# Kernel optimization log

Hardware: AMD Instinct MI355X
Metric: run time of the kernel (lower is better)

The kernel has to match this reference:

```python
import jax, jax.numpy as jnp
import numpy as np

B, CIN, COUT, H, W, K = 4, 64, 64, 128, 128, 3
KK = K * K


def setup_inputs() -> dict:
    key = jax.random.key(0)
    k = jax.random.split(key, 7)
    return {
        "input_feat": jax.random.normal(k[0], (B, CIN, H, W), jnp.float32),
        "inter": jax.random.normal(k[1], (B, CIN, H, W), jnp.float32),
        "fea": jax.random.normal(k[2], (B, 4 * CIN, 1, 1), jnp.float32),
        "weight": jax.random.uniform(k[3], (COUT, CIN, K, K), jnp.float32, -1.0, 1.0) / np.float32(np.sqrt(CIN * KK)),
        "bias": jnp.zeros((COUT,), jnp.float32),
        # conv_offset_mask params (torch zero-inits; small random values used so offsets/masks are non-trivial)
        "com_w": jax.random.normal(k[4], (3 * KK, CIN, K, K), jnp.float32) * 0.01,
        "com_b": jnp.zeros((3 * KK,), jnp.float32),
        "c1_w": jax.random.normal(k[5], (COUT, 4 * CIN), jnp.float32) / np.float32(np.sqrt(4 * CIN)),
        "c2_w": jax.random.normal(k[6], (COUT, COUT), jnp.float32) / np.float32(np.sqrt(COUT)),
    }


def reference(input_feat, inter, fea, weight, bias, com_w, com_b, c1_w, c2_w):
    b, c, h, w = input_feat.shape
    # offset/mask prediction: 3x3 conv, stride 1, pad 1 -> [b, 3*KK, h, w]
    om = jax.lax.conv_general_dilated(inter, com_w, (1, 1), ((1, 1), (1, 1)),
                                      dimension_numbers=("NCHW", "OIHW", "NCHW"))
    om = om + com_b[None, :, None, None]
    offset = jnp.concatenate([om[:, :KK], om[:, KK:2 * KK]], axis=1)  # [b, 2*KK, h, w]
    mask = jax.nn.sigmoid(om[:, 2 * KK:])                              # [b, KK, h, w]
    dy, dx = offset[:, 0::2], offset[:, 1::2]                          # mmcv interleaved (y, x) per tap

    # dynamic per-sample weight modulation (Cout == Cin, fea scales the in-channel axis)
    fvec = jnp.einsum('oc,bc->bo', c1_w, fea[:, :, 0, 0])              # [b, COUT]
    wdyn = weight[None] * fvec[:, None, :, None, None]                 # [b, COUT, CIN, K, K]

    # sampling coordinates: base grid (stride=1, pad=1, dil=1) + learned offsets
    ky = jnp.repeat(jnp.arange(K), K).astype(jnp.float32)              # [KK]
    kx = jnp.tile(jnp.arange(K), K).astype(jnp.float32)
    base_y = jnp.arange(h, dtype=jnp.float32)[None, :, None] - 1.0 + ky[:, None, None]  # [KK, h, 1]
    base_x = jnp.arange(w, dtype=jnp.float32)[None, None, :] - 1.0 + kx[:, None, None]  # [KK, 1, w]
    ys = base_y[None] + dy                                             # [b, KK, h, w]
    xs = base_x[None] + dx

    y0f = jnp.floor(ys); x0f = jnp.floor(xs)
    ly = ys - y0f; lx = xs - x0f
    y0 = y0f.astype(jnp.int32); x0 = x0f.astype(jnp.int32)
    xf = input_feat.reshape(b, c, h * w)

    def gather(yi, xi, wgt):
        valid = (yi >= 0) & (yi < h) & (xi >= 0) & (xi < w)
        idx = jnp.clip(yi, 0, h - 1) * w + jnp.clip(xi, 0, w - 1)      # [b, KK, h, w]
        v = jnp.take_along_axis(xf, idx.reshape(b, 1, -1), axis=2).reshape(b, c, KK, h, w)
        return v * (wgt * valid)[:, None]

    val = (gather(y0, x0, (1 - ly) * (1 - lx)) + gather(y0, x0 + 1, (1 - ly) * lx)
           + gather(y0 + 1, x0, ly * (1 - lx)) + gather(y0 + 1, x0 + 1, ly * lx))
    val = val * mask[:, None]                                          # modulated samples [b, c, KK, h, w]

    out = jnp.einsum('bocp,bcphw->bohw', wdyn.reshape(b, COUT, c, KK), val) + bias[None, :, None, None]
    return jnp.einsum('oc,bchw->bohw', c2_w, out)                      # c2: 1x1 conv, no bias
```

## Files before the change

### kernel.cpp

```cpp
#include <hip/hip_runtime.h>
#include <math.h>

#define BB 4
#define CIN 64
#define COUT 64
#define HH 128
#define WW 128
#define HW (HH*WW)

typedef __attribute__((ext_vector_type(8))) short short8;
typedef __attribute__((ext_vector_type(4))) float f32x4;
typedef __attribute__((ext_vector_type(4))) unsigned int uint4v;

static __device__ __forceinline__ unsigned short f2bf(float f) {
    unsigned int u = __builtin_bit_cast(unsigned int, f);
    u += 0x7fffu + ((u >> 16) & 1u);
    return (unsigned short)(u >> 16);
}
static __device__ __forceinline__ float bf2f(unsigned short h) {
    unsigned int u = ((unsigned int)h) << 16;
    return __builtin_bit_cast(float, u);
}

__global__ __launch_bounds__(256) void prep_kernel(
        const float* __restrict__ com_w, const float* __restrict__ c2w,
        const float* __restrict__ bias,
        unsigned short* __restrict__ wk2, float* __restrict__ bias2) {
    int id = blockIdx.x, tid = threadIdx.x;
    if (id < 80) {
        int i = id*256 + tid;
        int k = i & 31, oc = (i >> 5) & 31;
        int cc5 = i >> 10;
        int cg = cc5 / 5, ch = cc5 % 5;
        int tap = ch*2 + (k >> 4);
        int c = cg*16 + (k & 15);
        float v = 0.f;
        if (tap < 9 && oc < 27) v = com_w[((size_t)oc*64 + c)*9 + tap];
        wk2[i] = f2bf(v);
    } else if (tid < COUT) {
        float s2 = 0.f;
        for (int o = 0; o < COUT; ++o) s2 += c2w[tid*COUT + o] * bias[o];
        bias2[tid] = s2;
    }
}

static __device__ __forceinline__ void transpose_body(
        const float* __restrict__ srcb, unsigned short* __restrict__ dstb,
        int tb, int tid, float* lt ) {
    int b = tb >> 8;
    int px0 = (tb & 255) * 64;
    const float* src = srcb + (size_t)b*CIN*HW + px0;
    for (int i = tid; i < 4096; i += 256) {
        int c = i >> 6, px = i & 63;
        lt[c*65 + px] = src[(size_t)c*HW + px];
    }
    __syncthreads();
    int q = tid & 3, px = tid >> 2;
    unsigned short* dst = dstb + ((size_t)b*HW + px0 + px)*64 + q*16;
    #pragma unroll
    for (int s = 0; s < 2; ++s) {
        short8 pk;
        #pragma unroll
        for (int j = 0; j < 8; ++j)
            pk[j] = (short)f2bf(lt[(q*16 + s*8 + j)*65 + px]);
        *(short8*)(dst + s*8) = pk;
    }
}

static __device__ __forceinline__ void w2_body(
        int wid, int tid, const float* __restrict__ weight,
        const float* __restrict__ c2w, const float* __restrict__ c1w,
        const float* __restrict__ fea,
        unsigned short* __restrict__ w2b, float* c2s, float* wcol) {
    int o2 = tid & 63, ci = tid >> 6;
    int lane = tid & 63;
    int bp = wid >> 4;
    int c_base = (wid & 15)*4;
    int p = bp % 9, b = bp / 9;
    int c = c_base + ci;

    float part = 0.f;
    #pragma unroll
    for (int s = 0; s < 4; ++s)
        part += c1w[c*(4*CIN) + lane + s*64] * fea[b*(4*CIN) + lane + s*64];
    #pragma unroll
    for (int off = 32; off; off >>= 1) part += __shfl_down(part, off);
    float fv = __shfl(part, 0);

    for (int idx = tid; idx < 4096; idx += 256) {
        int o2r = idx >> 6, oc = idx & 63;
        c2s[oc*65 + o2r] = c2w[idx];
    }
    {
        int o = tid & 63, cw = tid >> 6;
        wcol[cw*64 + o] = weight[(o*CIN + (c_base + cw))*9 + p];
    }
    __syncthreads();
    float s = 0.f;
    #pragma unroll 8
    for (int o = 0; o < COUT; ++o) s += c2s[o*65 + o2] * wcol[ci*64 + o];
    w2b[(size_t)bp*4096 + o2*64 + (c ^ ((o2 & 7) << 3))] = f2bf(s * fv);
}

static __device__ __forceinline__ void conv_lds_body(
        int id, int tid, const float* __restrict__ inter,
        const unsigned short* __restrict__ wk2, const float* __restrict__ com_b,
        float* __restrict__ om, float* smemf) {
    unsigned short* til = (unsigned short*)smemf;
    int bz = id >> 6;
    int b = bz >> 1, mh = bz & 1;
    int by = (id >> 3) & 7, bx = id & 7;
    int x0 = bx*16, y0 = by*16;
    int lane = tid & 63, wv = tid >> 6;
    int nn = lane & 15, qq = lane >> 4;

    f32x4 acc[4];
    #pragma unroll
    for (int nt = 0; nt < 4; ++nt)
        #pragma unroll
        for (int j = 0; j < 4; ++j) acc[nt][j] = 0.f;

    for (int cg = 0; cg < 4; ++cg) {
        __syncthreads();
        const float* I = inter + ((size_t)(b*CIN + cg*16))*HW;
        for (int i = tid; i < 16*324; i += 256) {
            int cl = i / 324, px = i % 324;
            int r = px / 18, cc = px % 18;
            int gy = y0 + r - 1, gx = x0 + cc - 1;
            float v = 0.f;
            if (gy >= 0 && gy < HH && gx >= 0 && gx < WW)
                v = I[(size_t)cl*HW + gy*WW + gx];
            til[px*24 + cl] = f2bf(v);
        }
        if (tid < 24) til[324*24 + tid] = 0;
        __syncthreads();

        short8 afr[5];
        #pragma unroll
        for (int ch = 0; ch < 5; ++ch)
            afr[ch] = *(const short8*)(wk2 +
                (((size_t)(cg*5 + ch)*32 + mh*16 + nn)*32 + qq*8));
        #pragma unroll
        for (int nt = 0; nt < 4; ++nt) {
            int row = wv*4 + nt;
            #pragma unroll
            for (int ch = 0; ch < 5; ++ch) {
                int tap = ch*2 + (qq >> 1);
                int px_idx;
                if (tap > 8) px_idx = 324;
                else {
                    int ky = tap/3, kx = tap%3;
                    px_idx = (row + ky)*18 + (nn + kx);
                }
                short8 bfr = *(const short8*)(til + px_idx*24 + (qq&1)*8);
                acc[nt] = __builtin_amdgcn_mfma_f32_16x16x32_bf16(
                              afr[ch], bfr, acc[nt], 0, 0, 0);
            }
        }
    }

    float* op = om + (size_t)b*27*HW;
    #pragma unroll
    for (int nt = 0; nt < 4; ++nt) {
        int pix = (y0 + wv*4 + nt)*WW + x0 + nn;
        #pragma unroll
        for (int j = 0; j < 4; ++j) {
            int oc = mh*16 + qq*4 + j;
            if (oc < 27)
                op[(size_t)oc*HW + pix] = acc[nt][j] + com_b[oc];
        }
    }
}

__global__ __launch_bounds__(256) void main2_kernel(
        const float* __restrict__ input_feat,
        const float* __restrict__ inter,
        const unsigned short* __restrict__ wk2,
        const float* __restrict__ com_b,
        const float* __restrict__ weight,
        const float* __restrict__ c2w,
        const float* __restrict__ c1w,
        const float* __restrict__ fea,
        float* __restrict__ om, unsigned short* __restrict__ w2b,
        unsigned short* __restrict__ fT) {
    __shared__ __align__(16) float smem[4416];
    int id = blockIdx.x, tid = threadIdx.x;
    if (id < 512)        conv_lds_body(id, tid, inter, wk2, com_b, om, smem);
    else if (id < 1088)  w2_body(id - 512, tid, weight, c2w, c1w, fea, w2b,
                                 smem, smem + 64*65);
    else                 transpose_body(input_feat, fT, id - 1088, tid, smem);
}

__global__ __launch_bounds__(256) void dcn_main_kernel(
        const unsigned short* __restrict__ fT,
        const unsigned short* __restrict__ w2b,
        const float* __restrict__ bias2,
        const float* __restrict__ om,
        float* __restrict__ out) {
    __shared__ __align__(16) unsigned short aT[2][4096];
    int id = blockIdx.x;
    int xcd = id & 7;
    int jj  = id >> 3;
    int b   = xcd >> 1;
    int y   = jj & 127;
    int xq  = ((xcd & 1) << 1) | (jj >> 7);

    int t = threadIdx.x;
    int lane = t & 63, wv = t >> 6;
    int strip = wv >> 1, kh = wv & 1;
    int nn = lane & 15, qq = lane >> 4;
    int px0 = xq*32 + strip*16;
    int x = px0 + nn;
    int pix = y*WW + x;
    const unsigned short* Fb = fT + (size_t)b*HW*64;
    const float* omb = om + (size_t)b*27*HW;
    const unsigned short* w2src = w2b + (size_t)(b*9)*4096;
    int co = kh*32 + qq*8;

    char* aTc0 = (char*)aT[0];
    char* aTc1 = (char*)aT[1];
    int stOff = wv*2048 + lane*16;
    int rsw   = (nn & 7) << 4;
    int rbase = kh*64 + qq*16;

    f32x4 acc[4];
    #pragma unroll
    for (int mt = 0; mt < 4; ++mt)
        #pragma unroll
        for (int j = 0; j < 4; ++j)
            acc[mt][j] = kh ? bias2[mt*16 + qq*4 + j] : 0.f;

    {
        const char* s = (const char*)w2src;
        __builtin_amdgcn_global_load_lds(
            (const __attribute__((address_space(1))) void*)(s + stOff),
            (__attribute__((address_space(3))) void*)(aTc0 + wv*2048),
            16, 0, 0);
        __builtin_amdgcn_global_load_lds(
            (const __attribute__((address_space(1))) void*)(s + stOff + 1024),
            (__attribute__((address_space(3))) void*)(aTc0 + wv*2048 + 1024),
            16, 0, 0);
    }

    float omy = omb[pix];
    float omx = omb[(size_t)HW + pix];
    float omm = omb[(size_t)18*HW + pix];
    __syncthreads();

    #pragma unroll
    for (int p = 0; p < 9; ++p) {
        char* bufR = (p & 1) ? aTc1 : aTc0;
        char* bufW = (p & 1) ? aTc0 : aTc1;

        if (p < 8) {
            const char* s = (const char*)(w2src + (size_t)(p + 1)*4096);
            __builtin_amdgcn_global_load_lds(
                (const __attribute__((address_space(1))) void*)(s + stOff),
                (__attribute__((address_space(3))) void*)(bufW + wv*2048),
                16, 0, 0);
            __builtin_amdgcn_global_load_lds(
                (const __attribute__((address_space(1))) void*)(s + stOff + 1024),
                (__attribute__((address_space(3))) void*)(bufW + wv*2048 + 1024),
                16, 0, 0);
        }

        short8 afr[4];
        #pragma unroll
        for (int mt = 0; mt < 4; ++mt)
            afr[mt] = *(const short8*)(bufR +
                          (((mt*16 + nn)*128 + rbase) ^ rsw));

        float mv = 1.f / (1.f + expf(-omm));
        float ysv = (float)(y - 1 + p/3) + omy;
        float xsv = (float)(x - 1 + p%3) + omx;
        float y0f = floorf(ysv), x0f = floorf(xsv);
        float ly = ysv - y0f, lx = xsv - x0f;
        int y0 = (int)y0f, x0i = (int)x0f;
        int y1 = y0 + 1, x1 = x0i + 1;
        float vy0 = (y0 >= 0 && y0 < HH) ? 1.f : 0.f;
        float vy1 = (y1 >= 0 && y1 < HH) ? 1.f : 0.f;
        float vx0 = (x0i >= 0 && x0i < WW) ? 1.f : 0.f;
        float vx1 = (x1 >= 0 && x1 < WW) ? 1.f : 0.f;
        float w00 = (1.f-ly)*(1.f-lx)*mv * vy0*vx0;
        float w01 = (1.f-ly)*lx      *mv * vy0*vx1;
        float w10 = ly      *(1.f-lx)*mv * vy1*vx0;
        float w11 = ly      *lx      *mv * vy1*vx1;
        int y0c = min(max(y0,0),HH-1), y1c = min(max(y1,0),HH-1);
        int x0c = min(max(x0i,0),WW-1), x1c = min(max(x1,0),WW-1);
        int i00 = y0c*WW + x0c, i01 = y0c*WW + x1c;
        int i10 = y1c*WW + x0c, i11 = y1c*WW + x1c;

        if (p < 8) {
            omy = omb[(size_t)(2*p+2)*HW + pix];
            omx = omb[(size_t)(2*p+3)*HW + pix];
            omm = omb[(size_t)(19+p )*HW + pix];
        }

        short8 c00 = *(const short8*)(Fb + (size_t)i00*64 + co);
        short8 c01 = *(const short8*)(Fb + (size_t)i01*64 + co);
        short8 c10 = *(const short8*)(Fb + (size_t)i10*64 + co);
        short8 c11 = *(const short8*)(Fb + (size_t)i11*64 + co);

        unsigned int pw[4];
        #pragma unroll
        for (int jp = 0; jp < 4; ++jp) {
            float v0 = w00*bf2f((unsigned short)c00[2*jp])
                     + w01*bf2f((unsigned short)c01[2*jp])
                     + w10*bf2f((unsigned short)c10[2*jp])
                     + w11*bf2f((unsigned short)c11[2*jp]);
            float v1 = w00*bf2f((unsigned short)c00[2*jp+1])
                     + w01*bf2f((unsigned short)c01[2*jp+1])
                     + w10*bf2f((unsigned short)c10[2*jp+1])
                     + w11*bf2f((unsigned short)c11[2*jp+1]);
            pw[jp] = (unsigned int)f2bf(v0) | ((unsigned int)f2bf(v1) << 16);
        }
        uint4v u4 = {pw[0], pw[1], pw[2], pw[3]};
        short8 bfr = __builtin_bit_cast(short8, u4);

        #pragma unroll
        for (int mt = 0; mt < 4; ++mt)
            acc[mt] = __builtin_amdgcn_mfma_f32_16x16x32_bf16(
                          afr[mt], bfr, acc[mt], 0, 0, 0);

        __syncthreads();
    }

    float* red = (float*)aTc1;
    if (kh == 0) {
        #pragma unroll
        for (int mt = 0; mt < 4; ++mt)
            #pragma unroll
            for (int j = 0; j < 4; ++j)
                red[(mt*4 + j)*128 + strip*64 + lane] = acc[mt][j];
    }
    __syncthreads();
    if (kh == 1) {
        float* outp = out + (size_t)b*COUT*HW + (size_t)y*WW + px0 + nn;
        #pragma unroll
        for (int mt = 0; mt < 4; ++mt)
            #pragma unroll
            for (int j = 0; j < 4; ++j)
                outp[(size_t)(mt*16 + qq*4 + j)*HW] =
                    acc[mt][j] + red[(mt*4 + j)*128 + strip*64 + lane];
    }
}

extern "C" void kernel_launch(void* const* d_in, const int* in_sizes, int n_in,
                              void* d_out, int out_size, void* d_ws, size_t ws_size,
                              hipStream_t stream) {
    const float* input_feat = (const float*)d_in[0];
    const float* inter      = (const float*)d_in[1];
    const float* fea        = (const float*)d_in[2];
    const float* weight     = (const float*)d_in[3];
    const float* bias       = (const float*)d_in[4];
    const float* com_w      = (const float*)d_in[5];
    const float* com_b      = (const float*)d_in[6];
    const float* c1w        = (const float*)d_in[7];
    const float* c2w        = (const float*)d_in[8];
    float* out = (float*)d_out;

    float* ws    = (float*)d_ws;
    float* bias2 = ws + 256;
    unsigned short* w2b = (unsigned short*)(ws + 512);
    float* om    = ws + 512 + 73728;
    unsigned short* wk2 = (unsigned short*)(om + 1769472);
    unsigned short* fT  = wk2 + 20480;

    prep_kernel<<<81, 256, 0, stream>>>(com_w, c2w, bias, wk2, bias2);
    main2_kernel<<<2112, 256, 0, stream>>>(input_feat, inter, wk2, com_b,
                                           weight, c2w, c1w, fea, om, w2b, fT);
    dcn_main_kernel<<<2048, 256, 0, stream>>>(fT, w2b, bias2, om, out);
}
```

Baseline: 170.4 us.

## Compute both output-channel halves per block and vectorize conv tile staging

The offset/mask conv blocks now cover a 16x8 pixel tile and compute both 16-channel output halves in the same block, instead of splitting the halves across separate blocks. Each input halo tile is therefore staged into LDS once rather than twice, and each B fragment read from LDS feeds two MFMAs. The LDS staging loop drops the per-element div/mod indexing in favor of a column-per-thread loop with clamped addresses and multiplicative masks, plus a small pass for the two right-edge columns. The block count stays at 512, while the larger halo overhead of a shorter tile and the extra accumulators are the trade-off.

```diff
diff --git a/kernel.cpp b/kernel.cpp
--- a/kernel.cpp
+++ b/kernel.cpp
@@ -107,68 +107,100 @@
         const unsigned short* __restrict__ wk2, const float* __restrict__ com_b,
         float* __restrict__ om, float* smemf) {
     unsigned short* til = (unsigned short*)smemf;
-    int bz = id >> 6;
-    int b = bz >> 1, mh = bz & 1;
-    int by = (id >> 3) & 7, bx = id & 7;
-    int x0 = bx*16, y0 = by*16;
+    int b  = id >> 7;
+    int t7 = id & 127;
+    int by = t7 >> 3;
+    int bx = t7 & 7;
+    int x0 = bx*16, y0 = by*8;
     int lane = tid & 63, wv = tid >> 6;
     int nn = lane & 15, qq = lane >> 4;
 
-    f32x4 acc[4];
-    #pragma unroll
-    for (int nt = 0; nt < 4; ++nt)
-        #pragma unroll
-        for (int j = 0; j < 4; ++j) acc[nt][j] = 0.f;
+    if (tid < 24) til[180*24 + tid] = 0;
+
+    int scl = tid & 15, scc = tid >> 4;
+    int sgx  = x0 + scc - 1;
+    int sgxc = max(sgx, 0);
+    float sfx = ((unsigned)sgx < WW) ? 1.f : 0.f;
+
+    f32x4 acc[2][2];
+    #pragma unroll
+    for (int nt = 0; nt < 2; ++nt)
+        #pragma unroll
+        for (int mh = 0; mh < 2; ++mh)
+            #pragma unroll
+            for (int j = 0; j < 4; ++j) acc[nt][mh][j] = 0.f;
 
     for (int cg = 0; cg < 4; ++cg) {
         __syncthreads();
         const float* I = inter + ((size_t)(b*CIN + cg*16))*HW;
-        for (int i = tid; i < 16*324; i += 256) {
-            int cl = i / 324, px = i % 324;
-            int r = px / 18, cc = px % 18;
-            int gy = y0 + r - 1, gx = x0 + cc - 1;
-            float v = 0.f;
-            if (gy >= 0 && gy < HH && gx >= 0 && gx < WW)
-                v = I[(size_t)cl*HW + gy*WW + gx];
-            til[px*24 + cl] = f2bf(v);
-        }
-        if (tid < 24) til[324*24 + tid] = 0;
+
+        {
+            const float* colp = I + (size_t)scl*HW + sgxc;
+            unsigned short* tp = til + scc*24 + scl;
+            #pragma unroll
+            for (int r = 0; r < 10; ++r) {
+                int gy  = y0 + r - 1;
+                int gyc = min(max(gy, 0), HH-1);
+                float m = ((unsigned)gy < HH) ? sfx : 0.f;
+                float v = colp[(size_t)gyc*WW] * m;
+                tp[r*(18*24)] = f2bf(v);
+            }
+        }
+        #pragma unroll
+        for (int k = 0; k < 2; ++k) {
+            int i = k*256 + tid;
+            if (i < 320) {
+                int cl  = i & 15;
+                int ccb = (i >> 4) & 1;
+                int r   = i >> 5;
+                int gx  = x0 + 15 + ccb;
+                int gy  = y0 + r - 1;
+                int gxc = min(gx, WW-1);
+                int gyc = min(max(gy, 0), HH-1);
+                float m = (((unsigned)gy < HH) && ((unsigned)gx < WW)) ? 1.f : 0.f;
+                float v = I[(size_t)cl*HW + gyc*WW + gxc] * m;
+                til[(r*18 + 16 + ccb)*24 + cl] = f2bf(v);
+            }
+        }
         __syncthreads();
 
-        short8 afr[5];
-        #pragma unroll
-        for (int ch = 0; ch < 5; ++ch)
-            afr[ch] = *(const short8*)(wk2 +
-                (((size_t)(cg*5 + ch)*32 + mh*16 + nn)*32 + qq*8));
-        #pragma unroll
-        for (int nt = 0; nt < 4; ++nt) {
-            int row = wv*4 + nt;
-            #pragma unroll
-            for (int ch = 0; ch < 5; ++ch) {
-                int tap = ch*2 + (qq >> 1);
+        #pragma unroll
+        for (int ch = 0; ch < 5; ++ch) {
+            short8 a0 = *(const short8*)(wk2 +
+                (((size_t)(cg*5 + ch)*32 + nn)*32 + qq*8));
+            short8 a1 = *(const short8*)(wk2 +
+                (((size_t)(cg*5 + ch)*32 + 16 + nn)*32 + qq*8));
+            int tap = ch*2 + (qq >> 1);
+            #pragma unroll
+            for (int nt = 0; nt < 2; ++nt) {
+                int row = wv*2 + nt;
                 int px_idx;
-                if (tap > 8) px_idx = 324;
+                if (tap > 8) px_idx = 180;
                 else {
                     int ky = tap/3, kx = tap%3;
                     px_idx = (row + ky)*18 + (nn + kx);
                 }
                 short8 bfr = *(const short8*)(til + px_idx*24 + (qq&1)*8);
-                acc[nt] = __builtin_amdgcn_mfma_f32_16x16x32_bf16(
-                              afr[ch], bfr, acc[nt], 0, 0, 0);
+                acc[nt][0] = __builtin_amdgcn_mfma_f32_16x16x32_bf16(
+                                 a0, bfr, acc[nt][0], 0, 0, 0);
+                acc[nt][1] = __builtin_amdgcn_mfma_f32_16x16x32_bf16(
+                                 a1, bfr, acc[nt][1], 0, 0, 0);
             }
         }
     }
 
     float* op = om + (size_t)b*27*HW;
     #pragma unroll
-    for (int nt = 0; nt < 4; ++nt) {
-        int pix = (y0 + wv*4 + nt)*WW + x0 + nn;
-        #pragma unroll
-        for (int j = 0; j < 4; ++j) {
-            int oc = mh*16 + qq*4 + j;
-            if (oc < 27)
-                op[(size_t)oc*HW + pix] = acc[nt][j] + com_b[oc];
-        }
+    for (int nt = 0; nt < 2; ++nt) {
+        int pix = (y0 + wv*2 + nt)*WW + x0 + nn;
+        #pragma unroll
+        for (int mh = 0; mh < 2; ++mh)
+            #pragma unroll
+            for (int j = 0; j < 4; ++j) {
+                int oc = mh*16 + qq*4 + j;
+                if (oc < 27)
+                    op[(size_t)oc*HW + pix] = acc[nt][mh][j] + com_b[oc];
+            }
     }
 }
 
```

Result: faster. 151.4 us (-11.2%).
